# Kernel optimization log

Measured on AMD Instinct MI355X. Metric: run time of the kernel, lower is better.

The kernel has to match this reference:

```python
import jax, jax.numpy as jnp
import numpy as np

N_NODES = 50000
N_EDGES = 800000
F_IN = 256
HIDDEN = 64
HEADS = 4
N_CLASS = 40
NEG_SLOPE = 0.2


def gat_layer(x, src, dst, W, al, ar, b, heads, out_dim):
    # x: [N, Fin] -> h: [N, H, D]
    N = x.shape[0]
    h = (x @ W).reshape(N, heads, out_dim)
    el = jnp.sum(h * al, axis=-1)  # [N, H]
    er = jnp.sum(h * ar, axis=-1)  # [N, H]
    e = jax.nn.leaky_relu(el[src] + er[dst], NEG_SLOPE)  # [E, H]
    # segment softmax over incoming edges of each destination node
    emax = jax.ops.segment_max(e, dst, num_segments=N)  # [N, H] (-inf for empty, unused)
    ex = jnp.exp(e - emax[dst])
    esum = jax.ops.segment_sum(ex, dst, num_segments=N)
    alpha = ex / esum[dst]  # [E, H]; esum[dst] >= ex > 0 per existing edge
    msg = h[src] * alpha[:, :, None]  # [E, H, D]
    out = jax.ops.segment_sum(msg, dst, num_segments=N)  # [N, H, D]
    return out + b.reshape(1, heads, out_dim)


def setup_inputs() -> dict:
    key = jax.random.key(0)
    ks = jax.random.split(key, 16)
    x = jax.random.normal(ks[0], (N_NODES, F_IN), dtype=jnp.float32)
    edge_index = jax.random.randint(ks[1], (2, N_EDGES), 0, N_NODES, dtype=jnp.int64)
    s = 0.1
    return {
        "x": x,
        "edge_index": edge_index,
        "W1": jax.random.normal(ks[2], (F_IN, HEADS * HIDDEN), dtype=jnp.float32) * s,
        "al1": jax.random.normal(ks[3], (HEADS, HIDDEN), dtype=jnp.float32) * s,
        "ar1": jax.random.normal(ks[4], (HEADS, HIDDEN), dtype=jnp.float32) * s,
        "b1": jnp.zeros((HEADS * HIDDEN,), dtype=jnp.float32),
        "W2": jax.random.normal(ks[5], (HEADS * HIDDEN, HEADS * HIDDEN), dtype=jnp.float32) * s,
        "al2": jax.random.normal(ks[6], (HEADS, HIDDEN), dtype=jnp.float32) * s,
        "ar2": jax.random.normal(ks[7], (HEADS, HIDDEN), dtype=jnp.float32) * s,
        "b2": jnp.zeros((HEADS * HIDDEN,), dtype=jnp.float32),
        "W3": jax.random.normal(ks[8], (HEADS * HIDDEN, N_CLASS), dtype=jnp.float32) * s,
        "al3": jax.random.normal(ks[9], (1, N_CLASS), dtype=jnp.float32) * s,
        "ar3": jax.random.normal(ks[10], (1, N_CLASS), dtype=jnp.float32) * s,
        "b3": jnp.zeros((N_CLASS,), dtype=jnp.float32),
    }


def reference(x, edge_index, W1, al1, ar1, b1, W2, al2, ar2, b2, W3, al3, ar3, b3):
    src, dst = edge_index[0], edge_index[1]
    N = x.shape[0]
    # layer 1: GATConv -> flatten heads -> ELU
    h = gat_layer(x, src, dst, W1, al1, ar1, b1, HEADS, HIDDEN).reshape(N, -1)
    h = jax.nn.elu(h)
    # layer 2
    h = gat_layer(h, src, dst, W2, al2, ar2, b2, HEADS, HIDDEN).reshape(N, -1)
    h = jax.nn.elu(h)
    # layer 3: 1 head -> mean over head dim
    h = gat_layer(h, src, dst, W3, al3, ar3, b3, 1, N_CLASS).mean(axis=1)
    return jax.nn.log_softmax(h, axis=1)
```

## Files before the change

### kernel.cpp

```cpp
#include <hip/hip_runtime.h>
#include <hip/hip_bf16.h>
#include <math.h>

#define N_NODES 50000
#define N_EDGES 800000
#define NCLASS 40
#define MAXE 64

using f32x4 = __attribute__((ext_vector_type(4))) float;
using s16x8 = __attribute__((ext_vector_type(8))) short;

__global__ void detect_i64(const int* __restrict__ raw, int* __restrict__ flag) {
  int t = threadIdx.x;
  int v = raw[2 * t + 1];
  unsigned long long any = __ballot(v != 0);
  if (t == 0) flag[0] = (any == 0ULL) ? 1 : 0;
}

__global__ void count_raw(const int* __restrict__ raw, const int* __restrict__ flag,
                          int* __restrict__ deg) {
  int e = blockIdx.x * blockDim.x + threadIdx.x;
  if (e >= N_EDGES) return;
  int d = flag[0] ? raw[2 * N_EDGES + 2 * e] : raw[N_EDGES + e];
  atomicAdd(&deg[d], 1);
}

__global__ void scan_bsum(const int* __restrict__ deg, int* __restrict__ bsums) {
  __shared__ int sm[256];
  int t = threadIdx.x;
  int i = blockIdx.x * 256 + t;
  sm[t] = (i < N_NODES) ? deg[i] : 0;
  __syncthreads();
  for (int off = 128; off > 0; off >>= 1) {
    if (t < off) sm[t] += sm[t + off];
    __syncthreads();
  }
  if (t == 0) bsums[blockIdx.x] = sm[0];
}

__global__ void scan_offsets(int* __restrict__ bsums, int* __restrict__ rowp, int nb) {
  __shared__ int sm[256];
  int t = threadIdx.x;
  int v = (t < nb) ? bsums[t] : 0;
  sm[t] = v;
  __syncthreads();
  for (int off = 1; off < 256; off <<= 1) {
    int add = (t >= off) ? sm[t - off] : 0;
    __syncthreads();
    sm[t] += add;
    __syncthreads();
  }
  if (t < nb) bsums[t] = sm[t] - v;
  if (t == 0) rowp[N_NODES] = N_EDGES;
}

__global__ void scan_final(const int* __restrict__ deg, const int* __restrict__ bsums,
                           int* __restrict__ rowp, int* __restrict__ cursor) {
  __shared__ int sm[256];
  int t = threadIdx.x;
  int i = blockIdx.x * 256 + t;
  int v = (i < N_NODES) ? deg[i] : 0;
  sm[t] = v;
  __syncthreads();
  for (int off = 1; off < 256; off <<= 1) {
    int add = (t >= off) ? sm[t - off] : 0;
    __syncthreads();
    sm[t] += add;
    __syncthreads();
  }
  int excl = sm[t] - v + bsums[blockIdx.x];
  if (i < N_NODES) { rowp[i] = excl; cursor[i] = excl; }
}

__global__ void scatter_raw(const int* __restrict__ raw, const int* __restrict__ flag,
                            int* __restrict__ cursor, int* __restrict__ srcs) {
  int e = blockIdx.x * blockDim.x + threadIdx.x;
  if (e >= N_EDGES) return;
  int f = flag[0];
  int s = f ? raw[2 * e] : raw[e];
  int d = f ? raw[2 * N_EDGES + 2 * e] : raw[N_EDGES + e];
  int pos = atomicAdd(&cursor[d], 1);
  srcs[pos] = s;
}

__global__ void prep_w(const float* __restrict__ W1, const float* __restrict__ W2,
                       const float* __restrict__ W3,
                       __hip_bfloat16* __restrict__ WT1, __hip_bfloat16* __restrict__ WT2,
                       __hip_bfloat16* __restrict__ WT3) {
  int b = blockIdx.x, t = threadIdx.x;
  if (b < 256) {
    int id = b * 256 + t;
    int n = id >> 8, k = id & 255;
    WT1[n * 256 + k] = __float2bfloat16(W1[k * 256 + n]);
  } else if (b < 512) {
    int id = (b - 256) * 256 + t;
    int n = id >> 8, k = id & 255;
    WT2[n * 256 + k] = __float2bfloat16(W2[k * 256 + n]);
  } else {
    int id = (b - 512) * 256 + t;
    int n = id >> 8, k = id & 255;
    WT3[n * 256 + k] = (n < NCLASS) ? __float2bfloat16(W3[k * NCLASS + n]) : __float2bfloat16(0.f);
  }
}

__global__ void cast_x(const float* __restrict__ x, __hip_bfloat16* __restrict__ xb) {
  int id = blockIdx.x * 256 + threadIdx.x;
  float4 v = *reinterpret_cast<const float4*>(x + (size_t)id * 4);
  ushort4 u;
  __hip_bfloat16 b;
  b = __float2bfloat16(v.x); u.x = *(unsigned short*)&b;
  b = __float2bfloat16(v.y); u.y = *(unsigned short*)&b;
  b = __float2bfloat16(v.z); u.z = *(unsigned short*)&b;
  b = __float2bfloat16(v.w); u.w = *(unsigned short*)&b;
  *reinterpret_cast<ushort4*>((unsigned short*)xb + (size_t)id * 4) = u;
}

__global__ __launch_bounds__(256) void gemm_gat12(const __hip_bfloat16* __restrict__ A,
                                                  const __hip_bfloat16* __restrict__ WT,
                                                  const float* __restrict__ al,
                                                  const float* __restrict__ ar,
                                                  __hip_bfloat16* __restrict__ hb,
                                                  float* __restrict__ el,
                                                  float* __restrict__ er) {
  constexpr int MREP = 4, NREP = 4;
  __shared__ __align__(16) __hip_bfloat16 As[128][40];
  __shared__ __align__(16) __hip_bfloat16 Bs[128][40];

  int t = threadIdx.x;
  int lane = t & 63, wave = t >> 6;
  int wr = wave >> 1, wc = wave & 1;
  int row0 = blockIdx.x * 128, col0 = blockIdx.y * 128;
  int ln = lane & 15;
  int kc8 = (lane >> 4) * 8;

  f32x4 acc[MREP][NREP];
  const f32x4 fz = {0.f, 0.f, 0.f, 0.f};
#pragma unroll
  for (int m = 0; m < MREP; ++m)
#pragma unroll
    for (int n = 0; n < NREP; ++n) acc[m][n] = fz;

  for (int k0 = 0; k0 < 256; k0 += 32) {
#pragma unroll
    for (int it = 0; it < 2; ++it) {
      int c = t + it * 256;
      int r = c >> 2, kc = (c & 3) * 8;
      int grow = row0 + r;
      f32x4 v = fz;
      if (grow < N_NODES)
        v = *reinterpret_cast<const f32x4*>(A + (size_t)grow * 256 + k0 + kc);
      *reinterpret_cast<f32x4*>(&As[r][kc]) = v;
    }
#pragma unroll
    for (int it = 0; it < 2; ++it) {
      int c = t + it * 256;
      int r = c >> 2, kc = (c & 3) * 8;
      f32x4 v = *reinterpret_cast<const f32x4*>(WT + (size_t)(col0 + r) * 256 + k0 + kc);
      *reinterpret_cast<f32x4*>(&Bs[r][kc]) = v;
    }
    __syncthreads();
    s16x8 af[MREP], bfr[NREP];
#pragma unroll
    for (int m = 0; m < MREP; ++m)
      af[m] = *reinterpret_cast<const s16x8*>(&As[wr * 64 + m * 16 + ln][kc8]);
#pragma unroll
    for (int n = 0; n < NREP; ++n)
      bfr[n] = *reinterpret_cast<const s16x8*>(&Bs[wc * 64 + n * 16 + ln][kc8]);
#pragma unroll
    for (int m = 0; m < MREP; ++m)
#pragma unroll
      for (int n = 0; n < NREP; ++n)
        acc[m][n] = __builtin_amdgcn_mfma_f32_16x16x32_bf16(af[m], bfr[n], acc[m][n], 0, 0, 0);
    __syncthreads();
  }

  int head = blockIdx.y * 2 + wc;
  float alv[NREP], arv[NREP];
#pragma unroll
  for (int n = 0; n < NREP; ++n) {
    int c = head * 64 + n * 16 + ln;
    alv[n] = al[c];
    arv[n] = ar[c];
  }
#pragma unroll
  for (int m = 0; m < MREP; ++m) {
#pragma unroll
    for (int r = 0; r < 4; ++r) {
      int row = row0 + wr * 64 + m * 16 + (lane >> 4) * 4 + r;
      bool ok = row < N_NODES;
      float pl = 0.f, pr = 0.f;
#pragma unroll
      for (int n = 0; n < NREP; ++n) {
        float v = acc[m][n][r];
        pl += v * alv[n];
        pr += v * arv[n];
        if (ok) hb[(size_t)row * 256 + head * 64 + n * 16 + ln] = __float2bfloat16(v);
      }
      for (int off = 1; off < 16; off <<= 1) {
        pl += __shfl_xor(pl, off);
        pr += __shfl_xor(pr, off);
      }
      if (ln == 0 && ok) {
        el[row * 4 + head] = pl;
        er[row * 4 + head] = pr;
      }
    }
  }
}

__global__ __launch_bounds__(256) void gemm_gat3(const __hip_bfloat16* __restrict__ A,
                                                 const __hip_bfloat16* __restrict__ WT,
                                                 const float* __restrict__ al,
                                                 const float* __restrict__ ar,
                                                 __hip_bfloat16* __restrict__ h3b,
                                                 float* __restrict__ el3,
                                                 float* __restrict__ er3) {
  constexpr int MREP = 2, NREP = 4;
  __shared__ __align__(16) __hip_bfloat16 As[128][40];
  __shared__ __align__(16) __hip_bfloat16 Bs[64][40];

  int t = threadIdx.x;
  int lane = t & 63, wave = t >> 6;
  int row0 = blockIdx.x * 128;
  int ln = lane & 15;
  int kc8 = (lane >> 4) * 8;

  f32x4 acc[MREP][NREP];
  const f32x4 fz = {0.f, 0.f, 0.f, 0.f};
#pragma unroll
  for (int m = 0; m < MREP; ++m)
#pragma unroll
    for (int n = 0; n < NREP; ++n) acc[m][n] = fz;

  for (int k0 = 0; k0 < 256; k0 += 32) {
#pragma unroll
    for (int it = 0; it < 2; ++it) {
      int c = t + it * 256;
      int r = c >> 2, kc = (c & 3) * 8;
      int grow = row0 + r;
      f32x4 v = fz;
      if (grow < N_NODES)
        v = *reinterpret_cast<const f32x4*>(A + (size_t)grow * 256 + k0 + kc);
      *reinterpret_cast<f32x4*>(&As[r][kc]) = v;
    }
    {
      int c = t;
      int r = c >> 2, kc = (c & 3) * 8;
      f32x4 v = *reinterpret_cast<const f32x4*>(WT + (size_t)r * 256 + k0 + kc);
      *reinterpret_cast<f32x4*>(&Bs[r][kc]) = v;
    }
    __syncthreads();
    s16x8 af[MREP], bfr[NREP];
#pragma unroll
    for (int m = 0; m < MREP; ++m)
      af[m] = *reinterpret_cast<const s16x8*>(&As[wave * 32 + m * 16 + ln][kc8]);
#pragma unroll
    for (int n = 0; n < NREP; ++n)
      bfr[n] = *reinterpret_cast<const s16x8*>(&Bs[n * 16 + ln][kc8]);
#pragma unroll
    for (int m = 0; m < MREP; ++m)
#pragma unroll
      for (int n = 0; n < NREP; ++n)
        acc[m][n] = __builtin_amdgcn_mfma_f32_16x16x32_bf16(af[m], bfr[n], acc[m][n], 0, 0, 0);
    __syncthreads();
  }

  float alv[NREP], arv[NREP];
#pragma unroll
  for (int n = 0; n < NREP; ++n) {
    int c = n * 16 + ln;
    alv[n] = (c < NCLASS) ? al[c] : 0.f;
    arv[n] = (c < NCLASS) ? ar[c] : 0.f;
  }
#pragma unroll
  for (int m = 0; m < MREP; ++m) {
#pragma unroll
    for (int r = 0; r < 4; ++r) {
      int row = row0 + wave * 32 + m * 16 + (lane >> 4) * 4 + r;
      bool ok = row < N_NODES;
      float pl = 0.f, pr = 0.f;
#pragma unroll
      for (int n = 0; n < NREP; ++n) {
        float v = acc[m][n][r];
        pl += v * alv[n];
        pr += v * arv[n];
        if (ok) h3b[(size_t)row * 64 + n * 16 + ln] = __float2bfloat16(v);
      }
      for (int off = 1; off < 16; off <<= 1) {
        pl += __shfl_xor(pl, off);
        pr += __shfl_xor(pr, off);
      }
      if (ln == 0 && ok) {
        el3[row] = pl;
        er3[row] = pr;
      }
    }
  }
}

__global__ __launch_bounds__(128) void agg_fused(const __hip_bfloat16* __restrict__ hb,
                                                 const float* __restrict__ el,
                                                 const float* __restrict__ er,
                                                 const float* __restrict__ bias,
                                                 const int* __restrict__ rowp,
                                                 const int* __restrict__ srcs,
                                                 __hip_bfloat16* __restrict__ ob) {
  __shared__ float eld[2][MAXE * 4];
  int wv = threadIdx.x >> 6, lane = threadIdx.x & 63;
  int n = blockIdx.x * 2 + wv;
  float* ew = eld[wv];
  int i0 = rowp[n], deg = rowp[n + 1] - i0;
  float4 ern4 = *reinterpret_cast<const float4*>(er + (size_t)n * 4);
  float m0 = -1e30f, m1 = -1e30f, m2 = -1e30f, m3 = -1e30f;
  float l0 = 0.f, l1 = 0.f, l2 = 0.f, l3 = 0.f;
  for (int j = lane; j < deg; j += 64) {
    int s = srcs[i0 + j];
    float4 e4 = *reinterpret_cast<const float4*>(el + (size_t)s * 4);
    float e0 = e4.x + ern4.x; e0 = (e0 >= 0.f) ? e0 : 0.2f * e0;
    float e1 = e4.y + ern4.y; e1 = (e1 >= 0.f) ? e1 : 0.2f * e1;
    float e2 = e4.z + ern4.z; e2 = (e2 >= 0.f) ? e2 : 0.2f * e2;
    float e3 = e4.w + ern4.w; e3 = (e3 >= 0.f) ? e3 : 0.2f * e3;
    if (j < MAXE)
      *reinterpret_cast<float4*>(&ew[j * 4]) = make_float4(e0, e1, e2, e3);
    float nm;
    nm = fmaxf(m0, e0); l0 = l0 * __expf(m0 - nm) + __expf(e0 - nm); m0 = nm;
    nm = fmaxf(m1, e1); l1 = l1 * __expf(m1 - nm) + __expf(e1 - nm); m1 = nm;
    nm = fmaxf(m2, e2); l2 = l2 * __expf(m2 - nm) + __expf(e2 - nm); m2 = nm;
    nm = fmaxf(m3, e3); l3 = l3 * __expf(m3 - nm) + __expf(e3 - nm); m3 = nm;
  }
#pragma unroll
  for (int off = 1; off < 64; off <<= 1) {
    float mo, lo, nm;
    mo = __shfl_xor(m0, off); lo = __shfl_xor(l0, off);
    nm = fmaxf(m0, mo); l0 = l0 * __expf(m0 - nm) + lo * __expf(mo - nm); m0 = nm;
    mo = __shfl_xor(m1, off); lo = __shfl_xor(l1, off);
    nm = fmaxf(m1, mo); l1 = l1 * __expf(m1 - nm) + lo * __expf(mo - nm); m1 = nm;
    mo = __shfl_xor(m2, off); lo = __shfl_xor(l2, off);
    nm = fmaxf(m2, mo); l2 = l2 * __expf(m2 - nm) + lo * __expf(mo - nm); m2 = nm;
    mo = __shfl_xor(m3, off); lo = __shfl_xor(l3, off);
    nm = fmaxf(m3, mo); l3 = l3 * __expf(m3 - nm) + lo * __expf(mo - nm); m3 = nm;
  }
  float inv0 = (l0 > 0.f) ? (1.f / l0) : 0.f;
  float inv1 = (l1 > 0.f) ? (1.f / l1) : 0.f;
  float inv2 = (l2 > 0.f) ? (1.f / l2) : 0.f;
  float inv3 = (l3 > 0.f) ? (1.f / l3) : 0.f;
  __syncthreads();
  int ecount = ((deg < MAXE) ? deg : MAXE) * 4;
  {
    int hh = lane & 3;
    float mm = (hh == 0) ? m0 : (hh == 1) ? m1 : (hh == 2) ? m2 : m3;
    float iv = (hh == 0) ? inv0 : (hh == 1) ? inv1 : (hh == 2) ? inv2 : inv3;
    for (int k = lane; k < ecount; k += 64) ew[k] = __expf(ew[k] - mm) * iv;
  }
  __syncthreads();
  int head = lane >> 4;
  float mh = (head == 0) ? m0 : (head == 1) ? m1 : (head == 2) ? m2 : m3;
  float ivh = (head == 0) ? inv0 : (head == 1) ? inv1 : (head == 2) ? inv2 : inv3;
  float ernh = (head == 0) ? ern4.x : (head == 1) ? ern4.y : (head == 2) ? ern4.z : ern4.w;
  const uint2* hp = (const uint2*)hb;
  float4 A = make_float4(0.f, 0.f, 0.f, 0.f);
  float4 B = make_float4(0.f, 0.f, 0.f, 0.f);
  float4 C = make_float4(0.f, 0.f, 0.f, 0.f);
  float4 D = make_float4(0.f, 0.f, 0.f, 0.f);
  int j = 0;
  for (; j + 3 < deg; j += 4) {
    int s0 = srcs[i0 + j], s1 = srcs[i0 + j + 1], s2 = srcs[i0 + j + 2], s3 = srcs[i0 + j + 3];
    float w0, w1, w2, w3;
    if (j + 3 < MAXE) {
      w0 = ew[(j + 0) * 4 + head];
      w1 = ew[(j + 1) * 4 + head];
      w2 = ew[(j + 2) * 4 + head];
      w3 = ew[(j + 3) * 4 + head];
    } else {
      float e0 = el[s0 * 4 + head] + ernh; e0 = (e0 >= 0.f) ? e0 : 0.2f * e0;
      float e1 = el[s1 * 4 + head] + ernh; e1 = (e1 >= 0.f) ? e1 : 0.2f * e1;
      float e2 = el[s2 * 4 + head] + ernh; e2 = (e2 >= 0.f) ? e2 : 0.2f * e2;
      float e3 = el[s3 * 4 + head] + ernh; e3 = (e3 >= 0.f) ? e3 : 0.2f * e3;
      w0 = __expf(e0 - mh) * ivh;
      w1 = __expf(e1 - mh) * ivh;
      w2 = __expf(e2 - mh) * ivh;
      w3 = __expf(e3 - mh) * ivh;
    }
    uint2 h0 = hp[(size_t)s0 * 64 + lane];
    uint2 h1 = hp[(size_t)s1 * 64 + lane];
    uint2 h2 = hp[(size_t)s2 * 64 + lane];
    uint2 h3v = hp[(size_t)s3 * 64 + lane];
    A.x += w0 * __uint_as_float(h0.x << 16);
    A.y += w0 * __uint_as_float(h0.x & 0xffff0000u);
    A.z += w0 * __uint_as_float(h0.y << 16);
    A.w += w0 * __uint_as_float(h0.y & 0xffff0000u);
    B.x += w1 * __uint_as_float(h1.x << 16);
    B.y += w1 * __uint_as_float(h1.x & 0xffff0000u);
    B.z += w1 * __uint_as_float(h1.y << 16);
    B.w += w1 * __uint_as_float(h1.y & 0xffff0000u);
    C.x += w2 * __uint_as_float(h2.x << 16);
    C.y += w2 * __uint_as_float(h2.x & 0xffff0000u);
    C.z += w2 * __uint_as_float(h2.y << 16);
    C.w += w2 * __uint_as_float(h2.y & 0xffff0000u);
    D.x += w3 * __uint_as_float(h3v.x << 16);
    D.y += w3 * __uint_as_float(h3v.x & 0xffff0000u);
    D.z += w3 * __uint_as_float(h3v.y << 16);
    D.w += w3 * __uint_as_float(h3v.y & 0xffff0000u);
  }
  for (; j < deg; ++j) {
    int s0 = srcs[i0 + j];
    float w0;
    if (j < MAXE) {
      w0 = ew[j * 4 + head];
    } else {
      float e0 = el[s0 * 4 + head] + ernh; e0 = (e0 >= 0.f) ? e0 : 0.2f * e0;
      w0 = __expf(e0 - mh) * ivh;
    }
    uint2 h0 = hp[(size_t)s0 * 64 + lane];
    A.x += w0 * __uint_as_float(h0.x << 16);
    A.y += w0 * __uint_as_float(h0.x & 0xffff0000u);
    A.z += w0 * __uint_as_float(h0.y << 16);
    A.w += w0 * __uint_as_float(h0.y & 0xffff0000u);
  }
  float4 b4 = *reinterpret_cast<const float4*>(bias + (size_t)lane * 4);
  float r0 = (A.x + B.x) + (C.x + D.x) + b4.x;
  float r1 = (A.y + B.y) + (C.y + D.y) + b4.y;
  float r2 = (A.z + B.z) + (C.z + D.z) + b4.z;
  float r3 = (A.w + B.w) + (C.w + D.w) + b4.w;
  r0 = (r0 > 0.f) ? r0 : (__expf(r0) - 1.f);
  r1 = (r1 > 0.f) ? r1 : (__expf(r1) - 1.f);
  r2 = (r2 > 0.f) ? r2 : (__expf(r2) - 1.f);
  r3 = (r3 > 0.f) ? r3 : (__expf(r3) - 1.f);
  __hip_bfloat16 q0 = __float2bfloat16(r0), q1 = __float2bfloat16(r1);
  __hip_bfloat16 q2 = __float2bfloat16(r2), q3 = __float2bfloat16(r3);
  uint2 o;
  o.x = (unsigned int)(*(unsigned short*)&q0) | ((unsigned int)(*(unsigned short*)&q1) << 16);
  o.y = (unsigned int)(*(unsigned short*)&q2) | ((unsigned int)(*(unsigned short*)&q3) << 16);
  ((uint2*)ob)[(size_t)n * 64 + lane] = o;
}

__global__ __launch_bounds__(128) void agg_cls_fused(const __hip_bfloat16* __restrict__ h3b,
                                                     const float* __restrict__ el3,
                                                     const float* __restrict__ er3,
                                                     const float* __restrict__ bias,
                                                     const int* __restrict__ rowp,
                                                     const int* __restrict__ srcs,
                                                     float* __restrict__ out) {
  __shared__ float eldc[2][MAXE];
  int wv = threadIdx.x >> 6, lane = threadIdx.x & 63;
  int n = blockIdx.x * 2 + wv;
  float* ec = eldc[wv];
  int i0 = rowp[n], deg = rowp[n + 1] - i0;
  float ern = er3[n];
  float m = -1e30f, l = 0.f;
  for (int j = lane; j < deg; j += 64) {
    int s = srcs[i0 + j];
    float e = el3[s] + ern;
    e = (e >= 0.f) ? e : 0.2f * e;
    if (j < MAXE) ec[j] = e;
    float nm = fmaxf(m, e);
    l = l * __expf(m - nm) + __expf(e - nm);
    m = nm;
  }
#pragma unroll
  for (int off = 1; off < 64; off <<= 1) {
    float mo = __shfl_xor(m, off), lo = __shfl_xor(l, off);
    float nm = fmaxf(m, mo);
    l = l * __expf(m - nm) + lo * __expf(mo - nm);
    m = nm;
  }
  float inv = (l > 0.f) ? (1.f / l) : 0.f;
  __syncthreads();
  int ecount = (deg < MAXE) ? deg : MAXE;
  for (int k = lane; k < ecount; k += 64) ec[k] = __expf(ec[k] - m) * inv;
  __syncthreads();
  bool act2 = lane < ((NCLASS + 1) / 2);
  const unsigned int* hp3 = (const unsigned int*)h3b;
  float ax = 0.f, ay = 0.f, bx = 0.f, by = 0.f;
  int j = 0;
  for (; j + 1 < deg; j += 2) {
    int s0 = srcs[i0 + j], s1 = srcs[i0 + j + 1];
    float w0, w1;
    if (j + 1 < MAXE) {
      w0 = ec[j];
      w1 = ec[j + 1];
    } else {
      float e0 = el3[s0] + ern; e0 = (e0 >= 0.f) ? e0 : 0.2f * e0;
      float e1 = el3[s1] + ern; e1 = (e1 >= 0.f) ? e1 : 0.2f * e1;
      w0 = __expf(e0 - m) * inv;
      w1 = __expf(e1 - m) * inv;
    }
    if (act2) {
      unsigned int h0 = hp3[(size_t)s0 * 32 + lane];
      unsigned int h1 = hp3[(size_t)s1 * 32 + lane];
      ax += w0 * __uint_as_float(h0 << 16);
      ay += w0 * __uint_as_float(h0 & 0xffff0000u);
      bx += w1 * __uint_as_float(h1 << 16);
      by += w1 * __uint_as_float(h1 & 0xffff0000u);
    }
  }
  if (j < deg) {
    int s0 = srcs[i0 + j];
    float w0;
    if (j < MAXE) {
      w0 = ec[j];
    } else {
      float e0 = el3[s0] + ern; e0 = (e0 >= 0.f) ? e0 : 0.2f * e0;
      w0 = __expf(e0 - m) * inv;
    }
    if (act2) {
      unsigned int h0 = hp3[(size_t)s0 * 32 + lane];
      ax += w0 * __uint_as_float(h0 << 16);
      ay += w0 * __uint_as_float(h0 & 0xffff0000u);
    }
  }
  float z0 = ax + bx + (act2 ? bias[2 * lane] : 0.f);
  float z1 = ay + by + (act2 ? bias[2 * lane + 1] : 0.f);
  float mx = act2 ? fmaxf(z0, z1) : -1e30f;
  for (int off = 32; off > 0; off >>= 1) mx = fmaxf(mx, __shfl_xor(mx, off));
  float sm = act2 ? (__expf(z0 - mx) + __expf(z1 - mx)) : 0.f;
  for (int off = 32; off > 0; off >>= 1) sm += __shfl_xor(sm, off);
  float ls = __logf(sm);
  if (act2) {
    float2 r;
    r.x = z0 - mx - ls;
    r.y = z1 - mx - ls;
    *reinterpret_cast<float2*>(out + (size_t)n * NCLASS + 2 * lane) = r;
  }
}

extern "C" void kernel_launch(void* const* d_in, const int* in_sizes, int n_in,
                              void* d_out, int out_size, void* d_ws, size_t ws_size,
                              hipStream_t stream) {
  const float* x   = (const float*)d_in[0];
  const int* edges = (const int*)d_in[1];
  const float* W1  = (const float*)d_in[2];
  const float* al1 = (const float*)d_in[3];
  const float* ar1 = (const float*)d_in[4];
  const float* b1  = (const float*)d_in[5];
  const float* W2  = (const float*)d_in[6];
  const float* al2 = (const float*)d_in[7];
  const float* ar2 = (const float*)d_in[8];
  const float* b2  = (const float*)d_in[9];
  const float* W3  = (const float*)d_in[10];
  const float* al3 = (const float*)d_in[11];
  const float* ar3 = (const float*)d_in[12];
  const float* b3  = (const float*)d_in[13];
  float* out = (float*)d_out;

  const size_t N = N_NODES, E = N_EDGES;
  float* el  = (float*)d_ws;
  float* er  = el + N * 4;
  float* el3 = er + N * 4;
  float* er3 = el3 + N;
  __hip_bfloat16* xb = (__hip_bfloat16*)(er3 + N);
  __hip_bfloat16* hb = xb + N * 256;
  __hip_bfloat16* ob = hb + N * 256;
  __hip_bfloat16* h3b = ob + N * 256;
  __hip_bfloat16* WT1 = h3b + N * 64;
  __hip_bfloat16* WT2 = WT1 + 256 * 256;
  __hip_bfloat16* WT3 = WT2 + 256 * 256;
  int* rowp   = (int*)(WT3 + 64 * 256);
  int* cursor = rowp + (N + 1);
  int* srcs   = cursor + N;
  int* deg    = srcs + E;
  int* bsums  = deg + N;
  int* flag   = bsums + 256;

  hipMemsetAsync(deg, 0, N * sizeof(int), stream);
  detect_i64<<<1, 64, 0, stream>>>(edges, flag);
  int eb = (int)((E + 255) / 256);
  count_raw<<<eb, 256, 0, stream>>>(edges, flag, deg);
  int nb = (int)((N + 255) / 256);
  scan_bsum<<<nb, 256, 0, stream>>>(deg, bsums);
  scan_offsets<<<1, 256, 0, stream>>>(bsums, rowp, nb);
  scan_final<<<nb, 256, 0, stream>>>(deg, bsums, rowp, cursor);
  scatter_raw<<<eb, 256, 0, stream>>>(edges, flag, cursor, srcs);

  cast_x<<<(unsigned)(N * 256 / 4 / 256), 256, 0, stream>>>(x, xb);
  prep_w<<<576, 256, 0, stream>>>(W1, W2, W3, WT1, WT2, WT3);

  dim3 gg((unsigned)((N + 127) / 128), 2);
  dim3 g3((unsigned)((N + 127) / 128), 1);

  gemm_gat12<<<gg, 256, 0, stream>>>(xb, WT1, al1, ar1, hb, el, er);
  agg_fused<<<(unsigned)(N / 2), 128, 0, stream>>>(hb, el, er, b1, rowp, srcs, ob);
  gemm_gat12<<<gg, 256, 0, stream>>>(ob, WT2, al2, ar2, hb, el, er);
  agg_fused<<<(unsigned)(N / 2), 128, 0, stream>>>(hb, el, er, b2, rowp, srcs, ob);
  gemm_gat3<<<g3, 256, 0, stream>>>(ob, WT3, al3, ar3, h3b, el3, er3);
  agg_cls_fused<<<(unsigned)(N / 2), 128, 0, stream>>>(h3b, el3, er3, b3, rowp, srcs, out);
}
```

Measured before the change: 487.0 us.

## Use two-pass max/sum softmax, defer normalization, and compact edge indices to int32

The aggregation kernels replace the online softmax (an exp rescale per edge and per shuffle step) with a max-only first pass, then an exponential-sum pass that writes unnormalized weights into shared memory. This drops one shared-memory pass and one barrier. Division by the sum moves to the end, applied once per output element. Edge preprocessing now writes compact int32 src/dst arrays in the counting kernel, so the scatter kernel reads those instead of re-decoding the raw, possibly int64, edge array. The cost is extra workspace and an extra write of both edge arrays.

```diff
diff --git a/kernel.cpp b/kernel.cpp
--- a/kernel.cpp
+++ b/kernel.cpp
@@ -17,11 +17,21 @@
   if (t == 0) flag[0] = (any == 0ULL) ? 1 : 0;
 }
 
-__global__ void count_raw(const int* __restrict__ raw, const int* __restrict__ flag,
-                          int* __restrict__ deg) {
+__global__ void norm_count(const int* __restrict__ raw, const int* __restrict__ flag,
+                           int* __restrict__ s32, int* __restrict__ d32,
+                           int* __restrict__ deg) {
   int e = blockIdx.x * blockDim.x + threadIdx.x;
   if (e >= N_EDGES) return;
-  int d = flag[0] ? raw[2 * N_EDGES + 2 * e] : raw[N_EDGES + e];
+  int s, d;
+  if (flag[0]) {
+    s = raw[2 * e];
+    d = raw[2 * N_EDGES + 2 * e];
+  } else {
+    s = raw[e];
+    d = raw[N_EDGES + e];
+  }
+  s32[e] = s;
+  d32[e] = d;
   atomicAdd(&deg[d], 1);
 }
 
@@ -72,15 +82,13 @@
   if (i < N_NODES) { rowp[i] = excl; cursor[i] = excl; }
 }
 
-__global__ void scatter_raw(const int* __restrict__ raw, const int* __restrict__ flag,
-                            int* __restrict__ cursor, int* __restrict__ srcs) {
+__global__ void scatter_edges(const int* __restrict__ s32, const int* __restrict__ d32,
+                              int* __restrict__ cursor, int* __restrict__ srcs) {
   int e = blockIdx.x * blockDim.x + threadIdx.x;
   if (e >= N_EDGES) return;
-  int f = flag[0];
-  int s = f ? raw[2 * e] : raw[e];
-  int d = f ? raw[2 * N_EDGES + 2 * e] : raw[N_EDGES + e];
+  int d = d32[e];
   int pos = atomicAdd(&cursor[d], 1);
-  srcs[pos] = s;
+  srcs[pos] = s32[e];
 }
 
 __global__ void prep_w(const float* __restrict__ W1, const float* __restrict__ W2,
@@ -312,46 +320,68 @@
   int i0 = rowp[n], deg = rowp[n + 1] - i0;
   float4 ern4 = *reinterpret_cast<const float4*>(er + (size_t)n * 4);
   float m0 = -1e30f, m1 = -1e30f, m2 = -1e30f, m3 = -1e30f;
-  float l0 = 0.f, l1 = 0.f, l2 = 0.f, l3 = 0.f;
+  float e0 = 0.f, e1 = 0.f, e2 = 0.f, e3 = 0.f;
   for (int j = lane; j < deg; j += 64) {
     int s = srcs[i0 + j];
     float4 e4 = *reinterpret_cast<const float4*>(el + (size_t)s * 4);
-    float e0 = e4.x + ern4.x; e0 = (e0 >= 0.f) ? e0 : 0.2f * e0;
-    float e1 = e4.y + ern4.y; e1 = (e1 >= 0.f) ? e1 : 0.2f * e1;
-    float e2 = e4.z + ern4.z; e2 = (e2 >= 0.f) ? e2 : 0.2f * e2;
-    float e3 = e4.w + ern4.w; e3 = (e3 >= 0.f) ? e3 : 0.2f * e3;
+    e0 = e4.x + ern4.x; e0 = (e0 >= 0.f) ? e0 : 0.2f * e0;
+    e1 = e4.y + ern4.y; e1 = (e1 >= 0.f) ? e1 : 0.2f * e1;
+    e2 = e4.z + ern4.z; e2 = (e2 >= 0.f) ? e2 : 0.2f * e2;
+    e3 = e4.w + ern4.w; e3 = (e3 >= 0.f) ? e3 : 0.2f * e3;
     if (j < MAXE)
       *reinterpret_cast<float4*>(&ew[j * 4]) = make_float4(e0, e1, e2, e3);
-    float nm;
-    nm = fmaxf(m0, e0); l0 = l0 * __expf(m0 - nm) + __expf(e0 - nm); m0 = nm;
-    nm = fmaxf(m1, e1); l1 = l1 * __expf(m1 - nm) + __expf(e1 - nm); m1 = nm;
-    nm = fmaxf(m2, e2); l2 = l2 * __expf(m2 - nm) + __expf(e2 - nm); m2 = nm;
-    nm = fmaxf(m3, e3); l3 = l3 * __expf(m3 - nm) + __expf(e3 - nm); m3 = nm;
+    m0 = fmaxf(m0, e0);
+    m1 = fmaxf(m1, e1);
+    m2 = fmaxf(m2, e2);
+    m3 = fmaxf(m3, e3);
   }
 #pragma unroll
   for (int off = 1; off < 64; off <<= 1) {
-    float mo, lo, nm;
-    mo = __shfl_xor(m0, off); lo = __shfl_xor(l0, off);
-    nm = fmaxf(m0, mo); l0 = l0 * __expf(m0 - nm) + lo * __expf(mo - nm); m0 = nm;
-    mo = __shfl_xor(m1, off); lo = __shfl_xor(l1, off);
-    nm = fmaxf(m1, mo); l1 = l1 * __expf(m1 - nm) + lo * __expf(mo - nm); m1 = nm;
-    mo = __shfl_xor(m2, off); lo = __shfl_xor(l2, off);
-    nm = fmaxf(m2, mo); l2 = l2 * __expf(m2 - nm) + lo * __expf(mo - nm); m2 = nm;
-    mo = __shfl_xor(m3, off); lo = __shfl_xor(l3, off);
-    nm = fmaxf(m3, mo); l3 = l3 * __expf(m3 - nm) + lo * __expf(mo - nm); m3 = nm;
+    m0 = fmaxf(m0, __shfl_xor(m0, off));
+    m1 = fmaxf(m1, __shfl_xor(m1, off));
+    m2 = fmaxf(m2, __shfl_xor(m2, off));
+    m3 = fmaxf(m3, __shfl_xor(m3, off));
+  }
+  float l0 = 0.f, l1 = 0.f, l2 = 0.f, l3 = 0.f;
+  if (deg <= 64) {
+    if (lane < deg) {
+      float w0 = __expf(e0 - m0), w1 = __expf(e1 - m1);
+      float w2 = __expf(e2 - m2), w3 = __expf(e3 - m3);
+      *reinterpret_cast<float4*>(&ew[lane * 4]) = make_float4(w0, w1, w2, w3);
+      l0 = w0; l1 = w1; l2 = w2; l3 = w3;
+    }
+  } else {
+    for (int j = lane; j < deg; j += 64) {
+      float a0, a1, a2, a3;
+      if (j < MAXE) {
+        float4 q = *reinterpret_cast<const float4*>(&ew[j * 4]);
+        a0 = q.x; a1 = q.y; a2 = q.z; a3 = q.w;
+      } else {
+        int s = srcs[i0 + j];
+        float4 q = *reinterpret_cast<const float4*>(el + (size_t)s * 4);
+        a0 = q.x + ern4.x; a0 = (a0 >= 0.f) ? a0 : 0.2f * a0;
+        a1 = q.y + ern4.y; a1 = (a1 >= 0.f) ? a1 : 0.2f * a1;
+        a2 = q.z + ern4.z; a2 = (a2 >= 0.f) ? a2 : 0.2f * a2;
+        a3 = q.w + ern4.w; a3 = (a3 >= 0.f) ? a3 : 0.2f * a3;
+      }
+      float w0 = __expf(a0 - m0), w1 = __expf(a1 - m1);
+      float w2 = __expf(a2 - m2), w3 = __expf(a3 - m3);
+      if (j < MAXE)
+        *reinterpret_cast<float4*>(&ew[j * 4]) = make_float4(w0, w1, w2, w3);
+      l0 += w0; l1 += w1; l2 += w2; l3 += w3;
+    }
+  }
+#pragma unroll
+  for (int off = 1; off < 64; off <<= 1) {
+    l0 += __shfl_xor(l0, off);
+    l1 += __shfl_xor(l1, off);
+    l2 += __shfl_xor(l2, off);
+    l3 += __shfl_xor(l3, off);
   }
   float inv0 = (l0 > 0.f) ? (1.f / l0) : 0.f;
   float inv1 = (l1 > 0.f) ? (1.f / l1) : 0.f;
   float inv2 = (l2 > 0.f) ? (1.f / l2) : 0.f;
   float inv3 = (l3 > 0.f) ? (1.f / l3) : 0.f;
-  __syncthreads();
-  int ecount = ((deg < MAXE) ? deg : MAXE) * 4;
-  {
-    int hh = lane & 3;
-    float mm = (hh == 0) ? m0 : (hh == 1) ? m1 : (hh == 2) ? m2 : m3;
-    float iv = (hh == 0) ? inv0 : (hh == 1) ? inv1 : (hh == 2) ? inv2 : inv3;
-    for (int k = lane; k < ecount; k += 64) ew[k] = __expf(ew[k] - mm) * iv;
-  }
   __syncthreads();
   int head = lane >> 4;
   float mh = (head == 0) ? m0 : (head == 1) ? m1 : (head == 2) ? m2 : m3;
@@ -372,14 +402,14 @@
       w2 = ew[(j + 2) * 4 + head];
       w3 = ew[(j + 3) * 4 + head];
     } else {
-      float e0 = el[s0 * 4 + head] + ernh; e0 = (e0 >= 0.f) ? e0 : 0.2f * e0;
-      float e1 = el[s1 * 4 + head] + ernh; e1 = (e1 >= 0.f) ? e1 : 0.2f * e1;
-      float e2 = el[s2 * 4 + head] + ernh; e2 = (e2 >= 0.f) ? e2 : 0.2f * e2;
-      float e3 = el[s3 * 4 + head] + ernh; e3 = (e3 >= 0.f) ? e3 : 0.2f * e3;
-      w0 = __expf(e0 - mh) * ivh;
-      w1 = __expf(e1 - mh) * ivh;
-      w2 = __expf(e2 - mh) * ivh;
-      w3 = __expf(e3 - mh) * ivh;
+      float q0 = el[s0 * 4 + head] + ernh; q0 = (q0 >= 0.f) ? q0 : 0.2f * q0;
+      float q1 = el[s1 * 4 + head] + ernh; q1 = (q1 >= 0.f) ? q1 : 0.2f * q1;
+      float q2 = el[s2 * 4 + head] + ernh; q2 = (q2 >= 0.f) ? q2 : 0.2f * q2;
+      float q3 = el[s3 * 4 + head] + ernh; q3 = (q3 >= 0.f) ? q3 : 0.2f * q3;
+      w0 = __expf(q0 - mh);
+      w1 = __expf(q1 - mh);
+      w2 = __expf(q2 - mh);
+      w3 = __expf(q3 - mh);
     }
     uint2 h0 = hp[(size_t)s0 * 64 + lane];
     uint2 h1 = hp[(size_t)s1 * 64 + lane];
@@ -408,8 +438,8 @@
     if (j < MAXE) {
       w0 = ew[j * 4 + head];
     } else {
-      float e0 = el[s0 * 4 + head] + ernh; e0 = (e0 >= 0.f) ? e0 : 0.2f * e0;
-      w0 = __expf(e0 - mh) * ivh;
+      float q0 = el[s0 * 4 + head] + ernh; q0 = (q0 >= 0.f) ? q0 : 0.2f * q0;
+      w0 = __expf(q0 - mh);
     }
     uint2 h0 = hp[(size_t)s0 * 64 + lane];
     A.x += w0 * __uint_as_float(h0.x << 16);
@@ -418,10 +448,10 @@
     A.w += w0 * __uint_as_float(h0.y & 0xffff0000u);
   }
   float4 b4 = *reinterpret_cast<const float4*>(bias + (size_t)lane * 4);
-  float r0 = (A.x + B.x) + (C.x + D.x) + b4.x;
-  float r1 = (A.y + B.y) + (C.y + D.y) + b4.y;
-  float r2 = (A.z + B.z) + (C.z + D.z) + b4.z;
-  float r3 = (A.w + B.w) + (C.w + D.w) + b4.w;
+  float r0 = ((A.x + B.x) + (C.x + D.x)) * ivh + b4.x;
+  float r1 = ((A.y + B.y) + (C.y + D.y)) * ivh + b4.y;
+  float r2 = ((A.z + B.z) + (C.z + D.z)) * ivh + b4.z;
+  float r3 = ((A.w + B.w) + (C.w + D.w)) * ivh + b4.w;
   r0 = (r0 > 0.f) ? r0 : (__expf(r0) - 1.f);
   r1 = (r1 > 0.f) ? r1 : (__expf(r1) - 1.f);
   r2 = (r2 > 0.f) ? r2 : (__expf(r2) - 1.f);
@@ -447,27 +477,41 @@
   float* ec = eldc[wv];
   int i0 = rowp[n], deg = rowp[n + 1] - i0;
   float ern = er3[n];
-  float m = -1e30f, l = 0.f;
+  float m = -1e30f, e = 0.f;
   for (int j = lane; j < deg; j += 64) {
     int s = srcs[i0 + j];
-    float e = el3[s] + ern;
+    e = el3[s] + ern;
     e = (e >= 0.f) ? e : 0.2f * e;
     if (j < MAXE) ec[j] = e;
-    float nm = fmaxf(m, e);
-    l = l * __expf(m - nm) + __expf(e - nm);
-    m = nm;
-  }
-#pragma unroll
-  for (int off = 1; off < 64; off <<= 1) {
-    float mo = __shfl_xor(m, off), lo = __shfl_xor(l, off);
-    float nm = fmaxf(m, mo);
-    l = l * __expf(m - nm) + lo * __expf(mo - nm);
-    m = nm;
-  }
+    m = fmaxf(m, e);
+  }
+#pragma unroll
+  for (int off = 1; off < 64; off <<= 1) m = fmaxf(m, __shfl_xor(m, off));
+  float l = 0.f;
+  if (deg <= 64) {
+    if (lane < deg) {
+      float w = __expf(e - m);
+      ec[lane] = w;
+      l = w;
+    }
+  } else {
+    for (int j = lane; j < deg; j += 64) {
+      float a;
+      if (j < MAXE) {
+        a = ec[j];
+      } else {
+        int s = srcs[i0 + j];
+        a = el3[s] + ern;
+        a = (a >= 0.f) ? a : 0.2f * a;
+      }
+      float w = __expf(a - m);
+      if (j < MAXE) ec[j] = w;
+      l += w;
+    }
+  }
+#pragma unroll
+  for (int off = 1; off < 64; off <<= 1) l += __shfl_xor(l, off);
   float inv = (l > 0.f) ? (1.f / l) : 0.f;
-  __syncthreads();
-  int ecount = (deg < MAXE) ? deg : MAXE;
-  for (int k = lane; k < ecount; k += 64) ec[k] = __expf(ec[k] - m) * inv;
   __syncthreads();
   bool act2 = lane < ((NCLASS + 1) / 2);
   const unsigned int* hp3 = (const unsigned int*)h3b;
@@ -480,10 +524,10 @@
       w0 = ec[j];
       w1 = ec[j + 1];
     } else {
-      float e0 = el3[s0] + ern; e0 = (e0 >= 0.f) ? e0 : 0.2f * e0;
-      float e1 = el3[s1] + ern; e1 = (e1 >= 0.f) ? e1 : 0.2f * e1;
-      w0 = __expf(e0 - m) * inv;
-      w1 = __expf(e1 - m) * inv;
+      float q0 = el3[s0] + ern; q0 = (q0 >= 0.f) ? q0 : 0.2f * q0;
+      float q1 = el3[s1] + ern; q1 = (q1 >= 0.f) ? q1 : 0.2f * q1;
+      w0 = __expf(q0 - m);
+      w1 = __expf(q1 - m);
     }
     if (act2) {
       unsigned int h0 = hp3[(size_t)s0 * 32 + lane];
@@ -500,8 +544,8 @@
     if (j < MAXE) {
       w0 = ec[j];
     } else {
-      float e0 = el3[s0] + ern; e0 = (e0 >= 0.f) ? e0 : 0.2f * e0;
-      w0 = __expf(e0 - m) * inv;
+      float q0 = el3[s0] + ern; q0 = (q0 >= 0.f) ? q0 : 0.2f * q0;
+      w0 = __expf(q0 - m);
     }
     if (act2) {
       unsigned int h0 = hp3[(size_t)s0 * 32 + lane];
@@ -509,8 +553,8 @@
       ay += w0 * __uint_as_float(h0 & 0xffff0000u);
     }
   }
-  float z0 = ax + bx + (act2 ? bias[2 * lane] : 0.f);
-  float z1 = ay + by + (act2 ? bias[2 * lane + 1] : 0.f);
+  float z0 = (ax + bx) * inv + (act2 ? bias[2 * lane] : 0.f);
+  float z1 = (ay + by) * inv + (act2 ? bias[2 * lane + 1] : 0.f);
   float mx = act2 ? fmaxf(z0, z1) : -1e30f;
   for (int off = 32; off > 0; off >>= 1) mx = fmaxf(mx, __shfl_xor(mx, off));
   float sm = act2 ? (__expf(z0 - mx) + __expf(z1 - mx)) : 0.f;
@@ -560,17 +604,19 @@
   int* srcs   = cursor + N;
   int* deg    = srcs + E;
   int* bsums  = deg + N;
-  int* flag   = bsums + 256;
+  int* s32    = bsums + 256;
+  int* d32    = s32 + E;
+  int* flag   = d32 + E;
 
   hipMemsetAsync(deg, 0, N * sizeof(int), stream);
   detect_i64<<<1, 64, 0, stream>>>(edges, flag);
   int eb = (int)((E + 255) / 256);
-  count_raw<<<eb, 256, 0, stream>>>(edges, flag, deg);
+  norm_count<<<eb, 256, 0, stream>>>(edges, flag, s32, d32, deg);
   int nb = (int)((N + 255) / 256);
   scan_bsum<<<nb, 256, 0, stream>>>(deg, bsums);
   scan_offsets<<<1, 256, 0, stream>>>(bsums, rowp, nb);
   scan_final<<<nb, 256, 0, stream>>>(deg, bsums, rowp, cursor);
-  scatter_raw<<<eb, 256, 0, stream>>>(edges, flag, cursor, srcs);
+  scatter_edges<<<eb, 256, 0, stream>>>(s32, d32, cursor, srcs);
 
   cast_x<<<(unsigned)(N * 256 / 4 / 256), 256, 0, stream>>>(x, xb);
   prep_w<<<576, 256, 0, stream>>>(W1, W2, W3, WT1, WT2, WT3);
```

Result: faster. 477.3 us (-2.0%).
